# Optimization experiments

Measured on AMD Instinct MI355X. Metric: run time of the kernel, lower is better.

## Reference

```python
import jax, jax.numpy as jnp
import numpy as np

N_USER, N_ITEM = 50000, 50000
IN_DIM, HID, OUT = 256, 128, 64
E = 200000


def setup_inputs() -> dict:
    key = jax.random.key(0)
    ks = jax.random.split(key, 16)
    inp = {
        "x_user": jax.random.normal(ks[0], (N_USER, IN_DIM), jnp.float32),
        "x_item": jax.random.normal(ks[1], (N_ITEM, IN_DIM), jnp.float32),
        "W_proj": jax.random.normal(ks[2], (IN_DIM, HID), jnp.float32) / np.sqrt(IN_DIM),
        "b_proj": jax.random.normal(ks[3], (HID,), jnp.float32) * 0.01,
        "al_uu": jax.random.normal(ks[4], (1,), jnp.float32),
        "ar_uu": jax.random.normal(ks[5], (1,), jnp.float32),
        "al_iu": jax.random.normal(ks[6], (1,), jnp.float32),
        "ar_iu": jax.random.normal(ks[7], (1,), jnp.float32),
        "al_ui": jax.random.normal(ks[8], (1,), jnp.float32),
        "ar_ui": jax.random.normal(ks[9], (1,), jnp.float32),
        "W_out": jax.random.normal(ks[10], (HID, OUT), jnp.float32) / np.sqrt(HID),
        "b_out": jax.random.normal(ks[11], (OUT,), jnp.float32) * 0.01,
        "edges_uu": jax.random.randint(ks[12], (E, 2), 0, N_USER, jnp.int32),
        "edges_iu": jax.random.randint(ks[13], (E, 2), 0, N_ITEM, jnp.int32),
        "edges_ui": jax.random.randint(ks[14], (E, 2), 0, N_USER, jnp.int32),
    }
    return inp


def reference(x_user, x_item, W_proj, b_proj, al_uu, ar_uu, al_iu, ar_iu,
              al_ui, ar_ui, W_out, b_out, edges_uu, edges_iu, edges_ui):
    # shared projection of every node type
    h_u = x_user @ W_proj + b_proj  # [N_user, HID]
    h_i = x_item @ W_proj + b_proj  # [N_item, HID]

    out_u = jnp.zeros_like(h_u)
    out_i = jnp.zeros_like(h_i)

    # relation (user, follows, user): gather-scale, scatter-add into dst users
    msg = h_u[edges_uu[:, 0]] * al_uu + h_u[edges_uu[:, 1]] * ar_uu  # [E, HID]
    out_u = out_u.at[edges_uu[:, 1]].add(msg)

    # relation (item, owned, user)
    msg = h_i[edges_iu[:, 0]] * al_iu + h_u[edges_iu[:, 1]] * ar_iu
    out_u = out_u.at[edges_iu[:, 1]].add(msg)

    # relation (user, owns, item)
    msg = h_u[edges_ui[:, 0]] * al_ui + h_i[edges_ui[:, 1]] * ar_ui
    out_i = out_i.at[edges_ui[:, 1]].add(msg)

    out_u = jax.nn.elu(out_u)
    out_i = jax.nn.elu(out_i)
    out_u = out_u @ W_out + b_out  # 'user' gets the output linear
    return out_u, out_i
```

## Files before the change

kernel.cpp:

```cpp
#include <hip/hip_runtime.h>
#include <hip/hip_bf16.h>

typedef short bf16x8 __attribute__((ext_vector_type(8)));
typedef float f32x4 __attribute__((ext_vector_type(4)));

#define N_USER 50000
#define N_ITEM 50000
#define IN_DIM 256
#define HID 128
#define OUT_DIM 64
#define NEDGE 200000
#define CAP 32
#define NSTRIP 3125
#define FILL_GRID 121
#define PROJ_GRID 391

__device__ __forceinline__ float bf2f(unsigned short u) {
    union { unsigned int i; float f; } v; v.i = ((unsigned int)u) << 16; return v.f;
}
__device__ __forceinline__ unsigned short f2bf(float f) {
    union { float f; unsigned int i; } v; v.f = f;
    return (unsigned short)((v.i + 0x7fffu + ((v.i >> 16) & 1u)) >> 16);
}
__device__ __forceinline__ unsigned int cvt_pk_bf16(float a, float b) {
    unsigned int r;
    asm("v_cvt_pk_bf16_f32 %0, %1, %2" : "=v"(r) : "v"(a), "v"(b));
    return r;
}
__device__ __forceinline__ float elu_f(float x) {
    return x > 0.f ? x : (__expf(x) - 1.f);
}

__global__ __launch_bounds__(256) void pack_w_kernel(
    const float* __restrict__ Wp, const float* __restrict__ Wo,
    unsigned short* __restrict__ Wpk, unsigned short* __restrict__ Wok,
    int* __restrict__ cnt)
{
    int bid = blockIdx.x;
    if (bid >= 20) {
        int idx = (bid - 20) * 256 + threadIdx.x;
        if (idx < 3 * N_USER) cnt[idx] = 0;
        return;
    }
    int t = bid * 256 + threadIdx.x;
    if (t < 4096) {
        int lane = t & 63, kb = (t >> 6) & 7, nt = t >> 9;
        int r = lane & 15, kg = lane >> 4;
        unsigned short o[8];
        #pragma unroll
        for (int j = 0; j < 8; ++j)
            o[j] = f2bf(Wp[(size_t)(kb * 32 + kg * 8 + j) * HID + nt * 16 + r]);
        for (int cp = 0; cp < 8; ++cp) {
            #pragma unroll
            for (int j = 0; j < 8; ++j) Wpk[cp * 32768 + t * 8 + j] = o[j];
        }
    } else if (t < 4096 + 1024) {
        int q = t - 4096;
        int lane = q & 63, kb = (q >> 6) & 3, nt = q >> 8;
        int r = lane & 15, kg = lane >> 4;
        unsigned short o[8];
        #pragma unroll
        for (int j = 0; j < 8; ++j)
            o[j] = f2bf(Wo[(size_t)(j * 16 + kb * 4 + kg) * OUT_DIM + nt * 16 + r]);
        #pragma unroll
        for (int j = 0; j < 8; ++j) Wok[q * 8 + j] = o[j];
    }
}

__global__ __launch_bounds__(1024, 4) void proj_kernel(
    const float* __restrict__ x_u, const float* __restrict__ x_i,
    const unsigned short* __restrict__ Wpk, const float* __restrict__ b,
    unsigned short* __restrict__ h_u, unsigned short* __restrict__ h_i,
    const int* __restrict__ e_uu, const int* __restrict__ e_iu,
    const int* __restrict__ e_ui, int* __restrict__ cnt,
    int* __restrict__ bkt8, int* __restrict__ bktx)
{
    __shared__ unsigned short lds[HID * IN_DIM];

    int tid = threadIdx.x;
    int bid = blockIdx.x;

    if (bid < FILL_GRID) {
        for (int g = bid * 1024 + tid; g < 3 * NEDGE; g += FILL_GRID * 1024) {
            int rel = g >= 2 * NEDGE ? 2 : (g >= NEDGE ? 1 : 0);
            const int* e = rel == 0 ? e_uu : (rel == 1 ? e_iu : e_ui);
            int eid = g - rel * NEDGE;
            int2 sd = *(const int2*)(e + 2 * (size_t)eid);
            size_t drow = (size_t)rel * N_USER + sd.y;
            int slot = atomicAdd(&cnt[drow], 1);
            if (slot < 8)        bkt8[drow * 8 + slot] = sd.x;
            else if (slot < CAP) bktx[drow * 24 + (slot - 8)] = sd.x;
        }
        return;
    }
    bid -= FILL_GRID;

    const int4* wsel = (const int4*)(Wpk + (size_t)(bid & 7) * 32768);
    int4 w0 = wsel[tid];
    int4 w1 = wsel[1024 + tid];
    int4 w2 = wsel[2048 + tid];
    int4 w3 = wsel[3072 + tid];

    int wave = tid >> 6;
    int lane = tid & 63;
    int strip = bid * 16 + wave;
    strip = min(strip, 2 * NSTRIP - 1);
    const float* x = x_u;
    unsigned short* h = h_u;
    if (strip >= NSTRIP) { strip -= NSTRIP; x = x_i; h = h_i; }

    int row0 = strip * 16;
    int r  = lane & 15;
    int kg = lane >> 4;

    bf16x8 a[8];
    const float* xrow = x + (size_t)(row0 + r) * IN_DIM;
    #pragma unroll
    for (int kb = 0; kb < 8; ++kb) {
        float4 v0 = *(const float4*)(xrow + kb * 32 + kg * 8);
        float4 v1 = *(const float4*)(xrow + kb * 32 + kg * 8 + 4);
        unsigned int* au = (unsigned int*)&a[kb];
        au[0] = cvt_pk_bf16(v0.x, v0.y);
        au[1] = cvt_pk_bf16(v0.z, v0.w);
        au[2] = cvt_pk_bf16(v1.x, v1.y);
        au[3] = cvt_pk_bf16(v1.z, v1.w);
    }

    ((int4*)lds)[tid]        = w0;
    ((int4*)lds)[1024 + tid] = w1;
    ((int4*)lds)[2048 + tid] = w2;
    ((int4*)lds)[3072 + tid] = w3;
    __syncthreads();

    float bias[8];
    #pragma unroll
    for (int nt = 0; nt < 8; ++nt) bias[nt] = b[nt * 16 + r];

    f32x4 c[8];
    #pragma unroll
    for (int nt = 0; nt < 8; ++nt) c[nt] = (f32x4){0.f, 0.f, 0.f, 0.f};

    const bf16x8* wl = (const bf16x8*)lds + lane;
    #pragma unroll
    for (int nt = 0; nt < 8; ++nt) {
        #pragma unroll
        for (int kb = 0; kb < 8; ++kb)
            c[nt] = __builtin_amdgcn_mfma_f32_16x16x32_bf16(a[kb], wl[(nt * 8 + kb) * 64], c[nt], 0, 0, 0);
    }

    #pragma unroll
    for (int i = 0; i < 4; ++i) {
        uint4 val;
        val.x = cvt_pk_bf16(c[0][i] + bias[0], c[1][i] + bias[1]);
        val.y = cvt_pk_bf16(c[2][i] + bias[2], c[3][i] + bias[3]);
        val.z = cvt_pk_bf16(c[4][i] + bias[4], c[5][i] + bias[5]);
        val.w = cvt_pk_bf16(c[6][i] + bias[6], c[7][i] + bias[7]);
        *(uint4*)(h + (size_t)(row0 + kg * 4 + i) * HID + r * 8) = val;
    }
}

__global__ __launch_bounds__(256, 4) void epilogue_kernel(
    const unsigned short* __restrict__ h_u, const unsigned short* __restrict__ h_i,
    const int* __restrict__ cnt, const int* __restrict__ bkt8, const int* __restrict__ bktx,
    const float* __restrict__ al_uu, const float* __restrict__ ar_uu,
    const float* __restrict__ al_iu, const float* __restrict__ ar_iu,
    const float* __restrict__ al_ui, const float* __restrict__ ar_ui,
    const unsigned short* __restrict__ Wok, const float* __restrict__ bo,
    float* __restrict__ out_u, float* __restrict__ out_i)
{
    __shared__ unsigned short gbuf[16 * HID];
    __shared__ unsigned short ldsW[OUT_DIM * HID];

    int tid  = threadIdx.x;
    int wave = tid >> 6;
    int lane = tid & 63;

    if (blockIdx.x >= NSTRIP) {
        int v = (blockIdx.x - NSTRIP) * 4 + wave;
        if (v >= N_ITEM) return;

        unsigned int hv = *(const unsigned int*)(h_i + (size_t)v * HID + lane * 2);

        int d = cnt[2 * N_USER + v];
        const int4* bq4 = (const int4*)(bkt8 + (2 * (size_t)N_USER + v) * 8);
        int4 qa = bq4[0], qb = bq4[1];
        int idx[8] = {qa.x, qa.y, qa.z, qa.w, qb.x, qb.y, qb.z, qb.w};

        unsigned int rr[8];
        #pragma unroll
        for (int j = 0; j < 8; ++j) {
            int s = j < d ? idx[j] : v;
            rr[j] = *(const unsigned int*)(h_u + (size_t)s * HID + lane * 2);
        }
        float s0 = 0.f, s1 = 0.f;
        #pragma unroll
        for (int j = 0; j < 8; ++j) {
            s0 += bf2f((unsigned short)rr[j]);
            s1 += bf2f((unsigned short)(rr[j] >> 16));
        }
        int n = min(d, 8);
        float over = (float)(8 - n);
        s0 -= over * bf2f((unsigned short)rr[7]);
        s1 -= over * bf2f((unsigned short)(rr[7] >> 16));
        if (d > 8) {
            int nn = min(d, CAP);
            const int* bq = bktx + (2 * (size_t)N_USER + v) * 24;
            for (int j = 8; j < nn; ++j) {
                unsigned int u = *(const unsigned int*)(h_u + (size_t)bq[j - 8] * HID + lane * 2);
                s0 += bf2f((unsigned short)u);
                s1 += bf2f((unsigned short)(u >> 16));
            }
        }

        float rscale = ar_ui[0] * (float)d;
        float o0 = elu_f(rscale * bf2f((unsigned short)hv) + al_ui[0] * s0);
        float o1 = elu_f(rscale * bf2f((unsigned short)(hv >> 16)) + al_ui[0] * s1);

        int r_pos = lane >> 2;
        int c0 = ((2 * lane) & 7) * 16 + r_pos;
        float* orow = out_i + (size_t)v * HID;
        orow[c0]      = o0;
        orow[c0 + 16] = o1;
        return;
    }

    int base = blockIdx.x * 16;

    #pragma unroll
    for (int it = 0; it < 4; ++it)
        ((int4*)ldsW)[it * 256 + tid] = ((const int4*)Wok)[it * 256 + tid];

    float aluu = al_uu[0], aruu = ar_uu[0], aliu = al_iu[0], ariu = ar_iu[0];

    #pragma unroll 1
    for (int q = 0; q < 4; ++q) {
        int vloc = wave * 4 + q;
        int v = base + vloc;

        unsigned int hv = *(const unsigned int*)(h_u + (size_t)v * HID + lane * 2);
        int d_uu = cnt[v];
        int d_iu = cnt[N_USER + v];

        const int4* b0 = (const int4*)(bkt8 + (size_t)v * 8);
        const int4* b1 = (const int4*)(bkt8 + ((size_t)N_USER + v) * 8);
        int4 q0a = b0[0], q0b = b0[1];
        int4 q1a = b1[0], q1b = b1[1];
        int idx0[8] = {q0a.x, q0a.y, q0a.z, q0a.w, q0b.x, q0b.y, q0b.z, q0b.w};
        int idx1[8] = {q1a.x, q1a.y, q1a.z, q1a.w, q1b.x, q1b.y, q1b.z, q1b.w};

        unsigned int ru[8], ri[8];
        #pragma unroll
        for (int j = 0; j < 8; ++j) {
            int s = j < d_uu ? idx0[j] : v;
            ru[j] = *(const unsigned int*)(h_u + (size_t)s * HID + lane * 2);
        }
        #pragma unroll
        for (int j = 0; j < 8; ++j) {
            int s = j < d_iu ? idx1[j] : v;
            ri[j] = *(const unsigned int*)(h_i + (size_t)s * HID + lane * 2);
        }
        float s0u = 0.f, s1u = 0.f, s0i = 0.f, s1i = 0.f;
        #pragma unroll
        for (int j = 0; j < 8; ++j) {
            s0u += bf2f((unsigned short)ru[j]);
            s1u += bf2f((unsigned short)(ru[j] >> 16));
            s0i += bf2f((unsigned short)ri[j]);
            s1i += bf2f((unsigned short)(ri[j] >> 16));
        }
        int nu = min(d_uu, 8), ni = min(d_iu, 8);
        float ovu = (float)(8 - nu), ovi = (float)(8 - ni);
        s0u -= ovu * bf2f((unsigned short)ru[7]);
        s1u -= ovu * bf2f((unsigned short)(ru[7] >> 16));
        s0i -= ovi * bf2f((unsigned short)ri[7]);
        s1i -= ovi * bf2f((unsigned short)(ri[7] >> 16));
        if (d_uu > 8) {
            int nn = min(d_uu, CAP);
            const int* bq = bktx + (size_t)v * 24;
            for (int j = 8; j < nn; ++j) {
                unsigned int u = *(const unsigned int*)(h_u + (size_t)bq[j - 8] * HID + lane * 2);
                s0u += bf2f((unsigned short)u);
                s1u += bf2f((unsigned short)(u >> 16));
            }
        }
        if (d_iu > 8) {
            int nn = min(d_iu, CAP);
            const int* bq = bktx + ((size_t)N_USER + v) * 24;
            for (int j = 8; j < nn; ++j) {
                unsigned int u = *(const unsigned int*)(h_i + (size_t)bq[j - 8] * HID + lane * 2);
                s0i += bf2f((unsigned short)u);
                s1i += bf2f((unsigned short)(u >> 16));
            }
        }

        float rscale = aruu * (float)d_uu + ariu * (float)d_iu;
        float acc0 = aluu * s0u + aliu * s0i + rscale * bf2f((unsigned short)hv);
        float acc1 = aluu * s1u + aliu * s1i + rscale * bf2f((unsigned short)(hv >> 16));

        unsigned int packed = cvt_pk_bf16(elu_f(acc0), elu_f(acc1));
        *(unsigned int*)((char*)gbuf + ((vloc * 256 + lane * 4) ^ ((vloc & 7) << 4))) = packed;
    }
    __syncthreads();

    if (wave == 0) {
        int r  = lane & 15;
        int kg = lane >> 4;

        bf16x8 a[4];
        #pragma unroll
        for (int kb = 0; kb < 4; ++kb)
            a[kb] = *(const bf16x8*)((const char*)gbuf +
                      (((r * 256) + kb * 64 + kg * 16) ^ ((r & 7) << 4)));

        const bf16x8* wl = (const bf16x8*)ldsW + lane;
        #pragma unroll
        for (int nt = 0; nt < 4; ++nt) {
            f32x4 c = {0.f, 0.f, 0.f, 0.f};
            #pragma unroll
            for (int kb = 0; kb < 4; ++kb)
                c = __builtin_amdgcn_mfma_f32_16x16x32_bf16(a[kb], wl[(nt * 4 + kb) * 64], c, 0, 0, 0);
            float bias = bo[nt * 16 + r];
            #pragma unroll
            for (int i = 0; i < 4; ++i)
                out_u[(size_t)(base + kg * 4 + i) * OUT_DIM + nt * 16 + r] = c[i] + bias;
        }
    }
}

extern "C" void kernel_launch(void* const* d_in, const int* in_sizes, int n_in,
                              void* d_out, int out_size, void* d_ws, size_t ws_size,
                              hipStream_t stream)
{
    const float* x_user = (const float*)d_in[0];
    const float* x_item = (const float*)d_in[1];
    const float* W_proj = (const float*)d_in[2];
    const float* b_proj = (const float*)d_in[3];
    const float* al_uu  = (const float*)d_in[4];
    const float* ar_uu  = (const float*)d_in[5];
    const float* al_iu  = (const float*)d_in[6];
    const float* ar_iu  = (const float*)d_in[7];
    const float* al_ui  = (const float*)d_in[8];
    const float* ar_ui  = (const float*)d_in[9];
    const float* W_out  = (const float*)d_in[10];
    const float* b_out  = (const float*)d_in[11];
    const int* edges_uu = (const int*)d_in[12];
    const int* edges_iu = (const int*)d_in[13];
    const int* edges_ui = (const int*)d_in[14];

    char* ws = (char*)d_ws;
    unsigned short* h_u = (unsigned short*)(ws);
    unsigned short* h_i = (unsigned short*)(ws + 12800000);
    unsigned short* Wpk = (unsigned short*)(ws + 25600000);
    unsigned short* Wok = (unsigned short*)(ws + 26124288);
    int* cnt            = (int*)(ws + 26140672);
    int* bkt8           = (int*)(ws + 26740672);
    int* bktx           = (int*)(ws + 31540672);

    float* out_u = (float*)d_out;
    float* out_i = out_u + (size_t)N_USER * OUT_DIM;

    dim3 blk(256);
    pack_w_kernel<<<dim3(606), blk, 0, stream>>>(W_proj, W_out, Wpk, Wok, cnt);

    proj_kernel<<<dim3(FILL_GRID + PROJ_GRID), dim3(1024), 0, stream>>>(
        x_user, x_item, Wpk, b_proj, h_u, h_i,
        edges_uu, edges_iu, edges_ui, cnt, bkt8, bktx);

    epilogue_kernel<<<dim3(NSTRIP + 12500), blk, 0, stream>>>(
        h_u, h_i, cnt, bkt8, bktx, al_uu, ar_uu, al_iu, ar_iu, al_ui, ar_ui,
        Wok, b_out, out_u, out_i);
}
```

Baseline: 85.69 us.

## Process two nodes per wave in epilogue to overlap gathers; memset counters

```diff
diff --git a/kernel.cpp b/kernel.cpp
--- a/kernel.cpp
+++ b/kernel.cpp
@@ -33,16 +33,9 @@
 
 __global__ __launch_bounds__(256) void pack_w_kernel(
     const float* __restrict__ Wp, const float* __restrict__ Wo,
-    unsigned short* __restrict__ Wpk, unsigned short* __restrict__ Wok,
-    int* __restrict__ cnt)
+    unsigned short* __restrict__ Wpk, unsigned short* __restrict__ Wok)
 {
-    int bid = blockIdx.x;
-    if (bid >= 20) {
-        int idx = (bid - 20) * 256 + threadIdx.x;
-        if (idx < 3 * N_USER) cnt[idx] = 0;
-        return;
-    }
-    int t = bid * 256 + threadIdx.x;
+    int t = blockIdx.x * 256 + threadIdx.x;
     if (t < 4096) {
         int lane = t & 63, kb = (t >> 6) & 7, nt = t >> 9;
         int r = lane & 15, kg = lane >> 4;
@@ -176,51 +169,62 @@
     int lane = tid & 63;
 
     if (blockIdx.x >= NSTRIP) {
-        int v = (blockIdx.x - NSTRIP) * 4 + wave;
-        if (v >= N_ITEM) return;
-
-        unsigned int hv = *(const unsigned int*)(h_i + (size_t)v * HID + lane * 2);
-
-        int d = cnt[2 * N_USER + v];
-        const int4* bq4 = (const int4*)(bkt8 + (2 * (size_t)N_USER + v) * 8);
-        int4 qa = bq4[0], qb = bq4[1];
-        int idx[8] = {qa.x, qa.y, qa.z, qa.w, qb.x, qb.y, qb.z, qb.w};
-
-        unsigned int rr[8];
-        #pragma unroll
-        for (int j = 0; j < 8; ++j) {
-            int s = j < d ? idx[j] : v;
-            rr[j] = *(const unsigned int*)(h_u + (size_t)s * HID + lane * 2);
-        }
-        float s0 = 0.f, s1 = 0.f;
-        #pragma unroll
-        for (int j = 0; j < 8; ++j) {
-            s0 += bf2f((unsigned short)rr[j]);
-            s1 += bf2f((unsigned short)(rr[j] >> 16));
-        }
-        int n = min(d, 8);
-        float over = (float)(8 - n);
-        s0 -= over * bf2f((unsigned short)rr[7]);
-        s1 -= over * bf2f((unsigned short)(rr[7] >> 16));
-        if (d > 8) {
-            int nn = min(d, CAP);
-            const int* bq = bktx + (2 * (size_t)N_USER + v) * 24;
-            for (int j = 8; j < nn; ++j) {
-                unsigned int u = *(const unsigned int*)(h_u + (size_t)bq[j - 8] * HID + lane * 2);
-                s0 += bf2f((unsigned short)u);
-                s1 += bf2f((unsigned short)(u >> 16));
-            }
-        }
-
-        float rscale = ar_ui[0] * (float)d;
-        float o0 = elu_f(rscale * bf2f((unsigned short)hv) + al_ui[0] * s0);
-        float o1 = elu_f(rscale * bf2f((unsigned short)(hv >> 16)) + al_ui[0] * s1);
-
-        int r_pos = lane >> 2;
-        int c0 = ((2 * lane) & 7) * 16 + r_pos;
-        float* orow = out_i + (size_t)v * HID;
-        orow[c0]      = o0;
-        orow[c0 + 16] = o1;
+        int vbase = (blockIdx.x - NSTRIP) * 8 + wave * 2;
+
+        unsigned int hv[2];
+        int d[2];
+        int idx[2][8];
+        #pragma unroll
+        for (int p = 0; p < 2; ++p) {
+            int v = vbase + p;
+            hv[p] = *(const unsigned int*)(h_i + (size_t)v * HID + lane * 2);
+            d[p]  = cnt[2 * N_USER + v];
+            const int4* bq4 = (const int4*)(bkt8 + (2 * (size_t)N_USER + v) * 8);
+            int4 qa = bq4[0], qb = bq4[1];
+            idx[p][0] = qa.x; idx[p][1] = qa.y; idx[p][2] = qa.z; idx[p][3] = qa.w;
+            idx[p][4] = qb.x; idx[p][5] = qb.y; idx[p][6] = qb.z; idx[p][7] = qb.w;
+        }
+        unsigned int rr[2][8];
+        #pragma unroll
+        for (int p = 0; p < 2; ++p) {
+            #pragma unroll
+            for (int j = 0; j < 8; ++j) {
+                int s = j < d[p] ? idx[p][j] : (vbase + p);
+                rr[p][j] = *(const unsigned int*)(h_u + (size_t)s * HID + lane * 2);
+            }
+        }
+        #pragma unroll
+        for (int p = 0; p < 2; ++p) {
+            int v = vbase + p;
+            float s0 = 0.f, s1 = 0.f;
+            #pragma unroll
+            for (int j = 0; j < 8; ++j) {
+                s0 += bf2f((unsigned short)rr[p][j]);
+                s1 += bf2f((unsigned short)(rr[p][j] >> 16));
+            }
+            int n = min(d[p], 8);
+            float over = (float)(8 - n);
+            s0 -= over * bf2f((unsigned short)rr[p][7]);
+            s1 -= over * bf2f((unsigned short)(rr[p][7] >> 16));
+            if (d[p] > 8) {
+                int nn = min(d[p], CAP);
+                const int* bq = bktx + (2 * (size_t)N_USER + v) * 24;
+                for (int j = 8; j < nn; ++j) {
+                    unsigned int u = *(const unsigned int*)(h_u + (size_t)bq[j - 8] * HID + lane * 2);
+                    s0 += bf2f((unsigned short)u);
+                    s1 += bf2f((unsigned short)(u >> 16));
+                }
+            }
+            float rscale = ar_ui[0] * (float)d[p];
+            float o0 = elu_f(rscale * bf2f((unsigned short)hv[p]) + al_ui[0] * s0);
+            float o1 = elu_f(rscale * bf2f((unsigned short)(hv[p] >> 16)) + al_ui[0] * s1);
+
+            int r_pos = lane >> 2;
+            int c0 = ((2 * lane) & 7) * 16 + r_pos;
+            float* orow = out_i + (size_t)v * HID;
+            orow[c0]      = o0;
+            orow[c0 + 16] = o1;
+        }
         return;
     }
 
@@ -233,71 +237,88 @@
     float aluu = al_uu[0], aruu = ar_uu[0], aliu = al_iu[0], ariu = ar_iu[0];
 
     #pragma unroll 1
-    for (int q = 0; q < 4; ++q) {
-        int vloc = wave * 4 + q;
-        int v = base + vloc;
-
-        unsigned int hv = *(const unsigned int*)(h_u + (size_t)v * HID + lane * 2);
-        int d_uu = cnt[v];
-        int d_iu = cnt[N_USER + v];
-
-        const int4* b0 = (const int4*)(bkt8 + (size_t)v * 8);
-        const int4* b1 = (const int4*)(bkt8 + ((size_t)N_USER + v) * 8);
-        int4 q0a = b0[0], q0b = b0[1];
-        int4 q1a = b1[0], q1b = b1[1];
-        int idx0[8] = {q0a.x, q0a.y, q0a.z, q0a.w, q0b.x, q0b.y, q0b.z, q0b.w};
-        int idx1[8] = {q1a.x, q1a.y, q1a.z, q1a.w, q1b.x, q1b.y, q1b.z, q1b.w};
-
-        unsigned int ru[8], ri[8];
-        #pragma unroll
-        for (int j = 0; j < 8; ++j) {
-            int s = j < d_uu ? idx0[j] : v;
-            ru[j] = *(const unsigned int*)(h_u + (size_t)s * HID + lane * 2);
-        }
-        #pragma unroll
-        for (int j = 0; j < 8; ++j) {
-            int s = j < d_iu ? idx1[j] : v;
-            ri[j] = *(const unsigned int*)(h_i + (size_t)s * HID + lane * 2);
-        }
-        float s0u = 0.f, s1u = 0.f, s0i = 0.f, s1i = 0.f;
-        #pragma unroll
-        for (int j = 0; j < 8; ++j) {
-            s0u += bf2f((unsigned short)ru[j]);
-            s1u += bf2f((unsigned short)(ru[j] >> 16));
-            s0i += bf2f((unsigned short)ri[j]);
-            s1i += bf2f((unsigned short)(ri[j] >> 16));
-        }
-        int nu = min(d_uu, 8), ni = min(d_iu, 8);
-        float ovu = (float)(8 - nu), ovi = (float)(8 - ni);
-        s0u -= ovu * bf2f((unsigned short)ru[7]);
-        s1u -= ovu * bf2f((unsigned short)(ru[7] >> 16));
-        s0i -= ovi * bf2f((unsigned short)ri[7]);
-        s1i -= ovi * bf2f((unsigned short)(ri[7] >> 16));
-        if (d_uu > 8) {
-            int nn = min(d_uu, CAP);
-            const int* bq = bktx + (size_t)v * 24;
-            for (int j = 8; j < nn; ++j) {
-                unsigned int u = *(const unsigned int*)(h_u + (size_t)bq[j - 8] * HID + lane * 2);
-                s0u += bf2f((unsigned short)u);
-                s1u += bf2f((unsigned short)(u >> 16));
-            }
-        }
-        if (d_iu > 8) {
-            int nn = min(d_iu, CAP);
-            const int* bq = bktx + ((size_t)N_USER + v) * 24;
-            for (int j = 8; j < nn; ++j) {
-                unsigned int u = *(const unsigned int*)(h_i + (size_t)bq[j - 8] * HID + lane * 2);
-                s0i += bf2f((unsigned short)u);
-                s1i += bf2f((unsigned short)(u >> 16));
-            }
-        }
-
-        float rscale = aruu * (float)d_uu + ariu * (float)d_iu;
-        float acc0 = aluu * s0u + aliu * s0i + rscale * bf2f((unsigned short)hv);
-        float acc1 = aluu * s1u + aliu * s1i + rscale * bf2f((unsigned short)(hv >> 16));
-
-        unsigned int packed = cvt_pk_bf16(elu_f(acc0), elu_f(acc1));
-        *(unsigned int*)((char*)gbuf + ((vloc * 256 + lane * 4) ^ ((vloc & 7) << 4))) = packed;
+    for (int qq = 0; qq < 2; ++qq) {
+        int vloc0 = wave * 4 + qq * 2;
+
+        unsigned int hv[2];
+        int duu[2], diu[2];
+        int idx0[2][8], idx1[2][8];
+        #pragma unroll
+        for (int p = 0; p < 2; ++p) {
+            int v = base + vloc0 + p;
+            hv[p]  = *(const unsigned int*)(h_u + (size_t)v * HID + lane * 2);
+            duu[p] = cnt[v];
+            diu[p] = cnt[N_USER + v];
+            const int4* b0 = (const int4*)(bkt8 + (size_t)v * 8);
+            const int4* b1 = (const int4*)(bkt8 + ((size_t)N_USER + v) * 8);
+            int4 q0a = b0[0], q0b = b0[1];
+            int4 q1a = b1[0], q1b = b1[1];
+            idx0[p][0] = q0a.x; idx0[p][1] = q0a.y; idx0[p][2] = q0a.z; idx0[p][3] = q0a.w;
+            idx0[p][4] = q0b.x; idx0[p][5] = q0b.y; idx0[p][6] = q0b.z; idx0[p][7] = q0b.w;
+            idx1[p][0] = q1a.x; idx1[p][1] = q1a.y; idx1[p][2] = q1a.z; idx1[p][3] = q1a.w;
+            idx1[p][4] = q1b.x; idx1[p][5] = q1b.y; idx1[p][6] = q1b.z; idx1[p][7] = q1b.w;
+        }
+
+        unsigned int ru[2][8], ri[2][8];
+        #pragma unroll
+        for (int p = 0; p < 2; ++p) {
+            int v = base + vloc0 + p;
+            #pragma unroll
+            for (int j = 0; j < 8; ++j) {
+                int s = j < duu[p] ? idx0[p][j] : v;
+                ru[p][j] = *(const unsigned int*)(h_u + (size_t)s * HID + lane * 2);
+            }
+            #pragma unroll
+            for (int j = 0; j < 8; ++j) {
+                int s = j < diu[p] ? idx1[p][j] : v;
+                ri[p][j] = *(const unsigned int*)(h_i + (size_t)s * HID + lane * 2);
+            }
+        }
+
+        #pragma unroll
+        for (int p = 0; p < 2; ++p) {
+            int v = base + vloc0 + p;
+            float s0u = 0.f, s1u = 0.f, s0i = 0.f, s1i = 0.f;
+            #pragma unroll
+            for (int j = 0; j < 8; ++j) {
+                s0u += bf2f((unsigned short)ru[p][j]);
+                s1u += bf2f((unsigned short)(ru[p][j] >> 16));
+                s0i += bf2f((unsigned short)ri[p][j]);
+                s1i += bf2f((unsigned short)(ri[p][j] >> 16));
+            }
+            int nu = min(duu[p], 8), ni = min(diu[p], 8);
+            float ovu = (float)(8 - nu), ovi = (float)(8 - ni);
+            s0u -= ovu * bf2f((unsigned short)ru[p][7]);
+            s1u -= ovu * bf2f((unsigned short)(ru[p][7] >> 16));
+            s0i -= ovi * bf2f((unsigned short)ri[p][7]);
+            s1i -= ovi * bf2f((unsigned short)(ri[p][7] >> 16));
+            if (duu[p] > 8) {
+                int nn = min(duu[p], CAP);
+                const int* bq = bktx + (size_t)v * 24;
+                for (int j = 8; j < nn; ++j) {
+                    unsigned int u = *(const unsigned int*)(h_u + (size_t)bq[j - 8] * HID + lane * 2);
+                    s0u += bf2f((unsigned short)u);
+                    s1u += bf2f((unsigned short)(u >> 16));
+                }
+            }
+            if (diu[p] > 8) {
+                int nn = min(diu[p], CAP);
+                const int* bq = bktx + ((size_t)N_USER + v) * 24;
+                for (int j = 8; j < nn; ++j) {
+                    unsigned int u = *(const unsigned int*)(h_i + (size_t)bq[j - 8] * HID + lane * 2);
+                    s0i += bf2f((unsigned short)u);
+                    s1i += bf2f((unsigned short)(u >> 16));
+                }
+            }
+
+            float rscale = aruu * (float)duu[p] + ariu * (float)diu[p];
+            float acc0 = aluu * s0u + aliu * s0i + rscale * bf2f((unsigned short)hv[p]);
+            float acc1 = aluu * s1u + aliu * s1i + rscale * bf2f((unsigned short)(hv[p] >> 16));
+
+            unsigned int packed = cvt_pk_bf16(elu_f(acc0), elu_f(acc1));
+            int vloc = vloc0 + p;
+            *(unsigned int*)((char*)gbuf + ((vloc * 256 + lane * 4) ^ ((vloc & 7) << 4))) = packed;
+        }
     }
     __syncthreads();
 
@@ -359,13 +380,14 @@
     float* out_i = out_u + (size_t)N_USER * OUT_DIM;
 
     dim3 blk(256);
-    pack_w_kernel<<<dim3(606), blk, 0, stream>>>(W_proj, W_out, Wpk, Wok, cnt);
+    hipMemsetAsync(cnt, 0, 3 * N_USER * sizeof(int), stream);
+    pack_w_kernel<<<dim3(20), blk, 0, stream>>>(W_proj, W_out, Wpk, Wok);
 
     proj_kernel<<<dim3(FILL_GRID + PROJ_GRID), dim3(1024), 0, stream>>>(
         x_user, x_item, Wpk, b_proj, h_u, h_i,
         edges_uu, edges_iu, edges_ui, cnt, bkt8, bktx);
 
-    epilogue_kernel<<<dim3(NSTRIP + 12500), blk, 0, stream>>>(
+    epilogue_kernel<<<dim3(NSTRIP + 6250), blk, 0, stream>>>(
         h_u, h_i, cnt, bkt8, bktx, al_uu, ar_uu, al_iu, ar_iu, al_ui, ar_ui,
         Wok, b_out, out_u, out_i);
 }
```

New measurement: 87.76 us. 1.02x slower.

## Read projection weights from global/L2 instead of LDS, use 256-thread blocks

Applied to the files above, without the earlier changes.

```diff
diff --git a/kernel.cpp b/kernel.cpp
--- a/kernel.cpp
+++ b/kernel.cpp
@@ -12,8 +12,8 @@
 #define NEDGE 200000
 #define CAP 32
 #define NSTRIP 3125
-#define FILL_GRID 121
-#define PROJ_GRID 391
+#define FILL_BLKS 2344
+#define PROJ_BLKS 1563
 
 __device__ __forceinline__ float bf2f(unsigned short u) {
     union { unsigned int i; float f; } v; v.i = ((unsigned int)u) << 16; return v.f;
@@ -33,16 +33,9 @@
 
 __global__ __launch_bounds__(256) void pack_w_kernel(
     const float* __restrict__ Wp, const float* __restrict__ Wo,
-    unsigned short* __restrict__ Wpk, unsigned short* __restrict__ Wok,
-    int* __restrict__ cnt)
+    unsigned short* __restrict__ Wpk, unsigned short* __restrict__ Wok)
 {
-    int bid = blockIdx.x;
-    if (bid >= 20) {
-        int idx = (bid - 20) * 256 + threadIdx.x;
-        if (idx < 3 * N_USER) cnt[idx] = 0;
-        return;
-    }
-    int t = bid * 256 + threadIdx.x;
+    int t = blockIdx.x * 256 + threadIdx.x;
     if (t < 4096) {
         int lane = t & 63, kb = (t >> 6) & 7, nt = t >> 9;
         int r = lane & 15, kg = lane >> 4;
@@ -67,7 +60,7 @@
     }
 }
 
-__global__ __launch_bounds__(1024, 4) void proj_kernel(
+__global__ __launch_bounds__(256, 3) void proj_kernel(
     const float* __restrict__ x_u, const float* __restrict__ x_i,
     const unsigned short* __restrict__ Wpk, const float* __restrict__ b,
     unsigned short* __restrict__ h_u, unsigned short* __restrict__ h_i,
@@ -75,13 +68,12 @@
     const int* __restrict__ e_ui, int* __restrict__ cnt,
     int* __restrict__ bkt8, int* __restrict__ bktx)
 {
-    __shared__ unsigned short lds[HID * IN_DIM];
-
     int tid = threadIdx.x;
     int bid = blockIdx.x;
 
-    if (bid < FILL_GRID) {
-        for (int g = bid * 1024 + tid; g < 3 * NEDGE; g += FILL_GRID * 1024) {
+    if (bid < FILL_BLKS) {
+        int g = bid * 256 + tid;
+        if (g < 3 * NEDGE) {
             int rel = g >= 2 * NEDGE ? 2 : (g >= NEDGE ? 1 : 0);
             const int* e = rel == 0 ? e_uu : (rel == 1 ? e_iu : e_ui);
             int eid = g - rel * NEDGE;
@@ -93,17 +85,10 @@
         }
         return;
     }
-    bid -= FILL_GRID;
-
-    const int4* wsel = (const int4*)(Wpk + (size_t)(bid & 7) * 32768);
-    int4 w0 = wsel[tid];
-    int4 w1 = wsel[1024 + tid];
-    int4 w2 = wsel[2048 + tid];
-    int4 w3 = wsel[3072 + tid];
 
     int wave = tid >> 6;
     int lane = tid & 63;
-    int strip = bid * 16 + wave;
+    int strip = (bid - FILL_BLKS) * 4 + wave;
     strip = min(strip, 2 * NSTRIP - 1);
     const float* x = x_u;
     unsigned short* h = h_u;
@@ -126,12 +111,6 @@
         au[3] = cvt_pk_bf16(v1.z, v1.w);
     }
 
-    ((int4*)lds)[tid]        = w0;
-    ((int4*)lds)[1024 + tid] = w1;
-    ((int4*)lds)[2048 + tid] = w2;
-    ((int4*)lds)[3072 + tid] = w3;
-    __syncthreads();
-
     float bias[8];
     #pragma unroll
     for (int nt = 0; nt < 8; ++nt) bias[nt] = b[nt * 16 + r];
@@ -140,12 +119,12 @@
     #pragma unroll
     for (int nt = 0; nt < 8; ++nt) c[nt] = (f32x4){0.f, 0.f, 0.f, 0.f};
 
-    const bf16x8* wl = (const bf16x8*)lds + lane;
+    const bf16x8* wf = (const bf16x8*)(Wpk + (size_t)(bid & 7) * 32768) + lane;
     #pragma unroll
     for (int nt = 0; nt < 8; ++nt) {
         #pragma unroll
         for (int kb = 0; kb < 8; ++kb)
-            c[nt] = __builtin_amdgcn_mfma_f32_16x16x32_bf16(a[kb], wl[(nt * 8 + kb) * 64], c[nt], 0, 0, 0);
+            c[nt] = __builtin_amdgcn_mfma_f32_16x16x32_bf16(a[kb], wf[(nt * 8 + kb) * 64], c[nt], 0, 0, 0);
     }
 
     #pragma unroll
@@ -359,9 +338,10 @@
     float* out_i = out_u + (size_t)N_USER * OUT_DIM;
 
     dim3 blk(256);
-    pack_w_kernel<<<dim3(606), blk, 0, stream>>>(W_proj, W_out, Wpk, Wok, cnt);
-
-    proj_kernel<<<dim3(FILL_GRID + PROJ_GRID), dim3(1024), 0, stream>>>(
+    hipMemsetAsync(cnt, 0, 3 * N_USER * sizeof(int), stream);
+    pack_w_kernel<<<dim3(20), blk, 0, stream>>>(W_proj, W_out, Wpk, Wok);
+
+    proj_kernel<<<dim3(FILL_BLKS + PROJ_BLKS), blk, 0, stream>>>(
         x_user, x_item, Wpk, b_proj, h_u, h_i,
         edges_uu, edges_iu, edges_ui, cnt, bkt8, bktx);
 
```

Result: slower. 116.5 us (+35.9%).
